# Kernel tuning notes

Measured on AMD Instinct MI355X. Metric: run time of the kernel, lower is better.

Reference implementation:

```python
import jax, jax.numpy as jnp
import numpy as np

N_SPINS = 64
BATCH = 1_000_000
N_COUPLINGS = N_SPINS * (N_SPINS - 1) // 2  # 2016


def setup_inputs() -> dict:
    key = jax.random.key(0)
    k1, k2, k3 = jax.random.split(key, 3)
    # Ising spins are +/-1; sample random +/-1 states (Bernoulli(0.5) mapped to {-1,+1})
    states = jnp.where(jax.random.bernoulli(k1, 0.5, (BATCH, N_SPINS)), 1.0, -1.0).astype(jnp.float32)
    couplings_sigma = 1.0 / N_SPINS
    couplings = (jax.random.normal(k2, (N_COUPLINGS,), dtype=jnp.float32) * couplings_sigma)
    fields = (jax.random.normal(k3, (N_SPINS,), dtype=jnp.float32) * (1.0 / couplings_sigma))
    return {"states": states, "couplings": couplings, "fields": fields}


def _coupling_matrix(couplings, n):
    # scatter lower-diagonal coupling vector into [n,n] matrix and symmetrize
    rows, cols = jnp.tril_indices(n, k=-1)
    M = jnp.zeros((n, n), dtype=couplings.dtype).at[rows, cols].set(couplings)
    return M + M.T


def reference(states, couplings, fields) -> jnp.ndarray:
    n = fields.shape[0]
    J = _coupling_matrix(couplings, n)            # [N, N] symmetric, zero diagonal
    # H_couplings[b] = s_b^T J s_b ; H_fields[b] = f . s_b
    Js = states @ J                               # [B, N]
    H_couplings = jnp.einsum("bi,bi->b", states, Js)
    H_fields = states @ fields                    # [B]
    return -H_couplings - H_fields
```

## Files before the change

kernel.cpp:

```cpp
#include <hip/hip_runtime.h>

#define NSPIN   64
#define BATCH_N 1000000
#define NTILES  (BATCH_N / 16)
#define NBLOCKS 3125
#define NWAVES  (NBLOCKS * 4)
#define TPW     (NTILES / NWAVES)

typedef __bf16 bf16x8 __attribute__((ext_vector_type(8)));
typedef float  f32x4  __attribute__((ext_vector_type(4)));

__global__ void build_J_kernel(const float* __restrict__ couplings,
                               __bf16* __restrict__ Jg) {
    int idx = blockIdx.x * blockDim.x + threadIdx.x;
    if (idx >= NSPIN * NSPIN) return;
    int r = idx >> 6, c = idx & 63;
    float v = 0.0f;
    if (r > c)      v = couplings[(r * (r - 1)) / 2 + c];
    else if (r < c) v = couplings[(c * (c - 1)) / 2 + r];
    Jg[idx] = (__bf16)v;
}

__device__ __forceinline__ unsigned fbits(float x) {
    union { float f; unsigned u; } cv; cv.f = x; return cv.u;
}
__device__ __forceinline__ unsigned pack2(float lo, float hi) {
    return __builtin_amdgcn_perm(fbits(hi), fbits(lo), 0x07060302u);
}

__device__ __forceinline__ void gload_lds16(const void* g, void* l) {
    __builtin_amdgcn_global_load_lds(
        (const __attribute__((address_space(1))) unsigned int*)g,
        (__attribute__((address_space(3))) unsigned int*)l, 16, 0, 0);
}

template<bool USE_WS>
__global__ __launch_bounds__(256, 4) void ham_kernel(
    const float* __restrict__ states,
    const float* __restrict__ couplings,
    const float* __restrict__ fields,
    const __bf16* __restrict__ Jg,
    float* __restrict__ out)
{
    __shared__ char smem[48 * 1024];

    const int lane = threadIdx.x & 63;
    const int wid  = threadIdx.x >> 6;
    const int lo16 = lane & 15;
    const int g4   = lane >> 4;
    const int gw   = blockIdx.x * 4 + wid;

    bf16x8 jf[4][2];
    if constexpr (USE_WS) {
#pragma unroll
        for (int nb = 0; nb < 4; ++nb)
#pragma unroll
            for (int kb = 0; kb < 2; ++kb)
                jf[nb][kb] = *(const bf16x8*)(Jg + (nb * 16 + lo16) * NSPIN + kb * 32 + g4 * 8);
    } else {
        __bf16* J = (__bf16*)smem;
        for (int i = threadIdx.x; i < NSPIN * NSPIN; i += 256) {
            int r = i >> 6, c = i & 63;
            float v = 0.0f;
            if (r > c)      v = couplings[(r * (r - 1)) / 2 + c];
            else if (r < c) v = couplings[(c * (c - 1)) / 2 + r];
            J[i] = (__bf16)v;
        }
        __syncthreads();
#pragma unroll
        for (int nb = 0; nb < 4; ++nb)
#pragma unroll
            for (int kb = 0; kb < 2; ++kb)
                jf[nb][kb] = *(const bf16x8*)(J + (nb * 16 + lo16) * NSPIN + kb * 32 + g4 * 8);
        __syncthreads();
    }

    f32x4 ffrag[4];
#pragma unroll
    for (int nb = 0; nb < 4; ++nb)
        ffrag[nb] = *(const f32x4*)(fields + nb * 16 + g4 * 4);

    char* mybuf = smem + wid * (3 * 4096);

    int srcoff[4];
#pragma unroll
    for (int j = 0; j < 4; ++j) {
        int row   = 4 * j + g4;
        int chunk = lo16 ^ (row & 7);
        srcoff[j] = row * 256 + chunk * 16;
    }

    const char* sbase = (const char*)states;
    auto stage = [&](int buf, int t) {
        const char* src = sbase + (size_t)t * 4096;
#pragma unroll
        for (int j = 0; j < 4; ++j)
            gload_lds16(src + srcoff[j], mybuf + buf * 4096 + j * 1024);
    };
    auto lds_at = [&](const char* B, int row, int c) -> const void* {
        return (const void*)(B + row * 256 + (c ^ ((row & 7) << 4)));
    };

    stage(0, gw);
    stage(1, gw + NWAVES);

#pragma unroll
    for (int i = 0; i < TPW; ++i) {
        const int t = gw + i * NWAVES;
        if (i + 2 < TPW) {
            stage((i + 2) % 3, t + 2 * NWAVES);
            asm volatile("s_waitcnt vmcnt(8)" ::: "memory");
        } else if (i + 2 == TPW) {
            asm volatile("s_waitcnt vmcnt(4)" ::: "memory");
        } else {
            asm volatile("s_waitcnt vmcnt(0)" ::: "memory");
        }
        __builtin_amdgcn_sched_barrier(0);

        const char* B = mybuf + (i % 3) * 4096;

        f32x4 a0 = *(const f32x4*)lds_at(B, lo16, g4 * 32);
        f32x4 a1 = *(const f32x4*)lds_at(B, lo16, g4 * 32 + 16);
        f32x4 a2 = *(const f32x4*)lds_at(B, lo16, 128 + g4 * 32);
        f32x4 a3 = *(const f32x4*)lds_at(B, lo16, 128 + g4 * 32 + 16);

        f32x4 rv[4];
#pragma unroll
        for (int nb = 0; nb < 4; ++nb)
            rv[nb] = *(const f32x4*)lds_at(B, lo16, nb * 64 + g4 * 16);

        union { bf16x8 v; unsigned u[4]; } af0, af1;
        af0.u[0] = pack2(a0[0], a0[1]);
        af0.u[1] = pack2(a0[2], a0[3]);
        af0.u[2] = pack2(a1[0], a1[1]);
        af0.u[3] = pack2(a1[2], a1[3]);
        af1.u[0] = pack2(a2[0], a2[1]);
        af1.u[1] = pack2(a2[2], a2[3]);
        af1.u[2] = pack2(a3[0], a3[1]);
        af1.u[3] = pack2(a3[2], a3[3]);

        f32x4 acc[4];
#pragma unroll
        for (int nb = 0; nb < 4; ++nb) acc[nb] = ffrag[nb];
#pragma unroll
        for (int nb = 0; nb < 4; ++nb) {
            acc[nb] = __builtin_amdgcn_mfma_f32_16x16x32_bf16(jf[nb][0], af0.v, acc[nb], 0, 0, 0);
            acc[nb] = __builtin_amdgcn_mfma_f32_16x16x32_bf16(jf[nb][1], af1.v, acc[nb], 0, 0, 0);
        }

        float p = 0.f;
#pragma unroll
        for (int nb = 0; nb < 4; ++nb) {
            p += rv[nb][0] * acc[nb][0];
            p += rv[nb][1] * acc[nb][1];
            p += rv[nb][2] * acc[nb][2];
            p += rv[nb][3] * acc[nb][3];
        }
        p += __shfl_xor(p, 16, 64);
        p += __shfl_xor(p, 32, 64);
        if (g4 == 0)
            out[t * 16 + lo16] = -p;
    }
}

extern "C" void kernel_launch(void* const* d_in, const int* in_sizes, int n_in,
                              void* d_out, int out_size, void* d_ws, size_t ws_size,
                              hipStream_t stream) {
    const float* states    = (const float*)d_in[0];
    const float* couplings = (const float*)d_in[1];
    const float* fields    = (const float*)d_in[2];
    float* out = (float*)d_out;

    if (ws_size >= NSPIN * NSPIN * sizeof(__bf16)) {
        __bf16* Jg = (__bf16*)d_ws;
        build_J_kernel<<<16, 256, 0, stream>>>(couplings, Jg);
        ham_kernel<true><<<NBLOCKS, 256, 0, stream>>>(states, couplings, fields, Jg, out);
    } else {
        ham_kernel<false><<<NBLOCKS, 256, 0, stream>>>(states, couplings, fields, nullptr, out);
    }
}
```

Before: 47.13 us.

## Switch to persistent grid-stride loop with fewer blocks and precomputed LDS offsets

Cuts the grid from 3125 blocks to 768 and replaces the fixed unrolled per-wave tile count with a runtime grid-stride loop. Each wave now works through more tiles, so the one-time J and fields loads are amortised and the triple-buffered prefetch pipeline stays in steady state for longer. Swizzled LDS offsets are computed once outside the loop. The cost is fewer waves in flight, which may not hide memory latency as well, plus loop overhead and an uneven tile split since 62500 tiles do not divide evenly across 3072 waves.

```diff
diff --git a/kernel.cpp b/kernel.cpp
--- a/kernel.cpp
+++ b/kernel.cpp
@@ -3,9 +3,8 @@
 #define NSPIN   64
 #define BATCH_N 1000000
 #define NTILES  (BATCH_N / 16)
-#define NBLOCKS 3125
-#define NWAVES  (NBLOCKS * 4)
-#define TPW     (NTILES / NWAVES)
+#define NBLOCKS 768
+#define SW      (NBLOCKS * 4)
 
 typedef __bf16 bf16x8 __attribute__((ext_vector_type(8)));
 typedef float  f32x4  __attribute__((ext_vector_type(4)));
@@ -97,37 +96,45 @@
         for (int j = 0; j < 4; ++j)
             gload_lds16(src + srcoff[j], mybuf + buf * 4096 + j * 1024);
     };
-    auto lds_at = [&](const char* B, int row, int c) -> const void* {
-        return (const void*)(B + row * 256 + (c ^ ((row & 7) << 4)));
-    };
+
+    const int sw  = (lo16 & 7) << 4;
+    const int rb  = lo16 * 256;
+    int aoff[4], roff[4];
+    aoff[0] = rb + ((g4 * 32)       ^ sw);
+    aoff[1] = rb + ((g4 * 32 + 16)  ^ sw);
+    aoff[2] = rb + ((128 + g4 * 32) ^ sw);
+    aoff[3] = rb + ((128 + g4 * 32 + 16) ^ sw);
+#pragma unroll
+    for (int nb = 0; nb < 4; ++nb)
+        roff[nb] = rb + ((nb * 64 + g4 * 16) ^ sw);
 
     stage(0, gw);
-    stage(1, gw + NWAVES);
+    stage(1, gw + SW);
 
-#pragma unroll
-    for (int i = 0; i < TPW; ++i) {
-        const int t = gw + i * NWAVES;
-        if (i + 2 < TPW) {
-            stage((i + 2) % 3, t + 2 * NWAVES);
+    int bi = 0;
+    for (int t = gw; t < NTILES; t += SW) {
+        int bi2 = bi + 2; if (bi2 >= 3) bi2 -= 3;
+        if (t + 2 * SW < NTILES) {
+            stage(bi2, t + 2 * SW);
             asm volatile("s_waitcnt vmcnt(8)" ::: "memory");
-        } else if (i + 2 == TPW) {
+        } else if (t + SW < NTILES) {
             asm volatile("s_waitcnt vmcnt(4)" ::: "memory");
         } else {
             asm volatile("s_waitcnt vmcnt(0)" ::: "memory");
         }
         __builtin_amdgcn_sched_barrier(0);
 
-        const char* B = mybuf + (i % 3) * 4096;
+        const char* B = mybuf + bi * 4096;
 
-        f32x4 a0 = *(const f32x4*)lds_at(B, lo16, g4 * 32);
-        f32x4 a1 = *(const f32x4*)lds_at(B, lo16, g4 * 32 + 16);
-        f32x4 a2 = *(const f32x4*)lds_at(B, lo16, 128 + g4 * 32);
-        f32x4 a3 = *(const f32x4*)lds_at(B, lo16, 128 + g4 * 32 + 16);
+        f32x4 a0 = *(const f32x4*)(B + aoff[0]);
+        f32x4 a1 = *(const f32x4*)(B + aoff[1]);
+        f32x4 a2 = *(const f32x4*)(B + aoff[2]);
+        f32x4 a3 = *(const f32x4*)(B + aoff[3]);
 
         f32x4 rv[4];
 #pragma unroll
         for (int nb = 0; nb < 4; ++nb)
-            rv[nb] = *(const f32x4*)lds_at(B, lo16, nb * 64 + g4 * 16);
+            rv[nb] = *(const f32x4*)(B + roff[nb]);
 
         union { bf16x8 v; unsigned u[4]; } af0, af1;
         af0.u[0] = pack2(a0[0], a0[1]);
@@ -160,6 +167,8 @@
         p += __shfl_xor(p, 32, 64);
         if (g4 == 0)
             out[t * 16 + lo16] = -p;
+
+        bi = (bi == 2) ? 0 : bi + 1;
     }
 }
 
```

New measurement: 47.88 us. No clear change (+1.6%).
